# Optimization experiments

Hardware: AMD Instinct MI355X
Metric: run time of the kernel (lower is better)

The kernel has to match this reference:

```python
import jax, jax.numpy as jnp
import numpy as np
import math

EPS = 1e-5
GN_GROUPS = 32


def conv2d(x, w, padding):
    # x: [B,C,H,W], w: [O,I,kh,kw]
    return jax.lax.conv_general_dilated(
        x, w, window_strides=(1, 1), padding=[(padding, padding)] * 2,
        dimension_numbers=("NCHW", "OIHW", "NCHW"))


def group_norm(x, weight, bias, groups=GN_GROUPS, eps=EPS):
    B, C, H, W = x.shape
    xg = x.reshape(B, groups, C // groups, H, W)
    mu = xg.mean(axis=(2, 3, 4), keepdims=True)
    var = xg.var(axis=(2, 3, 4), keepdims=True)
    xn = (xg - mu) * jax.lax.rsqrt(var + eps)
    xn = xn.reshape(B, C, H, W)
    return xn * weight[None, :, None, None] + bias[None, :, None, None]


def setup_inputs() -> dict:
    key = jax.random.key(0)
    ks = jax.random.split(key, 8)
    B, C, H, W = 8, 256, 80, 80
    init_gate = 0.99
    gate_bias_val = 0.5 * math.log((1 + init_gate) / (1 - init_gate))
    return {
        "x": jax.random.normal(ks[0], (B, C, H, W), dtype=jnp.float32),
        "w1": jax.random.normal(ks[1], (C, C, 3, 3), dtype=jnp.float32) * 0.01,
        "gn1_w": jnp.ones((C,), dtype=jnp.float32),
        "gn1_b": jnp.zeros((C,), dtype=jnp.float32),
        "w2": jax.random.normal(ks[2], (C, C, 3, 3), dtype=jnp.float32) * 0.01,
        "gn2_w": jnp.ones((C,), dtype=jnp.float32),
        "gn2_b": jnp.zeros((C,), dtype=jnp.float32),
        "gate_w": jax.random.normal(ks[3], (1, C, 1, 1), dtype=jnp.float32) * 0.01,
        "gate_b": jnp.full((1,), gate_bias_val, dtype=jnp.float32),
    }


def reference(x, w1, gn1_w, gn1_b, w2, gn2_w, gn2_b, gate_w, gate_b):
    # shortcut is identity (in_channels == out_channels, stride 1)
    shortcut = x
    # conv1 -> GN -> ReLU
    h = jax.nn.relu(group_norm(conv2d(x, w1, padding=1), gn1_w, gn1_b))
    # conv2 -> GN
    h = group_norm(conv2d(h, w2, padding=1), gn2_w, gn2_b)
    # SpatialGate: 1x1 conv on the original input, ReTanH activation
    g = conv2d(x, gate_w, padding=0) + gate_b[None, :, None, None]  # [B,1,H,W]
    gate = jnp.clip(jnp.tanh(g), 0.0, None)
    # num_groups == 1: encode/decode are identity reshapes; gate broadcasts over C
    out = h * gate
    return jax.nn.relu(out + shortcut)
```

## Files before the change

kernel.cpp:

```cpp
#include <hip/hip_runtime.h>
#include <math.h>

#define NB   8
#define NC   256
#define NH   80
#define NW   80
#define NHW  6400
#define GN_EPS 1e-5f

typedef __bf16 bf16;
typedef bf16 bf16x2 __attribute__((ext_vector_type(2)));
typedef bf16 bf16x4 __attribute__((ext_vector_type(4)));
typedef bf16 bf16x8 __attribute__((ext_vector_type(8)));
typedef float f32x4 __attribute__((ext_vector_type(4)));

typedef __attribute__((address_space(1))) void gvoid;
typedef __attribute__((address_space(3))) void lvoid;
__device__ __forceinline__ void glds16(const void* g, void* l) {
    __builtin_amdgcn_global_load_lds((const gvoid*)g, (lvoid*)l, 16, 0, 0);
}

#define AW_T   2048
#define AW_BUF 18432

__global__ __launch_bounds__(256) void prep_kernel(
    const float* __restrict__ x, bf16* __restrict__ xp,
    const float* __restrict__ gw, float* __restrict__ gpart,
    const float* __restrict__ w1, const float* __restrict__ w2,
    bf16* __restrict__ wA1, bf16* __restrict__ wA2, float* __restrict__ stats)
{
    int bid = blockIdx.x;
    int tid = threadIdx.x;
    if (bid >= 5120) {
        int blk = bid - 5120;
        if (blk == 0) {
            #pragma unroll
            for (int k = 0; k < 8; k++) stats[tid + k * 256] = 0.0f;
            return;
        }
        int rb = blk - 1;
        const float* w = (rb < 2304) ? w1 : w2;
        bf16* wA       = (rb < 2304) ? wA1 : wA2;
        int idx = (rb % 2304) * 256 + tid;
        int c8  = idx & 7;
        int n   = (idx >> 3) & 15;
        int qq  = (idx >> 7) & 3;
        int coq = (idx >> 9) & 15;
        int tc  = idx >> 13;
        int tap = tc % 9, chunk = tc / 9;
        int ci = chunk * 32 + qq * 8 + c8;
        int co = coq * 16 + n;
        wA[idx] = (bf16)w[(size_t)(co * 256 + ci) * 9 + tap];
        return;
    }
    __shared__ float tile[8][4][84];
    int rg  = bid % 20;
    int cib = (bid / 20) & 31;
    int b   = bid / 640;
    for (int e = tid; e < 2560; e += 256) {
        int c8 = e / 320, r2 = e - c8 * 320;
        int rr = r2 / 80, col = r2 - rr * 80;
        tile[c8][rr][col] =
            x[((size_t)(b * NC + cib * 8 + c8) * NH + rg * 4 + rr) * NW + col];
    }
    __syncthreads();
    for (int t = tid; t < 1280; t += 256) {
        int rr = t / 320, t2 = t - rr * 320;
        int e = 2 * t2, col = e >> 3, c8 = e & 7;
        bf16x2 pk = { (bf16)tile[c8][rr][col], (bf16)tile[c8 + 1][rr][col] };
        size_t base = (((size_t)(b * 32 + cib) * 82 + rg * 4 + rr + 1) * 82) * 8 + 8;
        *(bf16x2*)(xp + base + e) = pk;
    }
    if (tid < 320) {
        int rr = tid / 80, col = tid - rr * 80;
        float s = 0.0f;
        #pragma unroll
        for (int c8 = 0; c8 < 8; c8++)
            s = fmaf(tile[c8][rr][col], gw[cib * 8 + c8], s);
        gpart[((size_t)cib * NB + b) * NHW + (rg * 4 + rr) * 80 + col] = s;
    }
    const uint4 z4 = make_uint4(0u, 0u, 0u, 0u);
    size_t img = ((size_t)(b * 32 + cib)) * 82;
    if (tid < 8) {
        int rr = tid >> 1, col = (tid & 1) * 81;
        *(uint4*)(xp + ((img + rg * 4 + rr + 1) * 82 + col) * 8) = z4;
    }
    if (rg == 0 || rg == 19) {
        int prow = (rg == 0) ? 0 : 81;
        for (int u = tid; u < 82; u += 256)
            *(uint4*)(xp + ((img + prow) * 82 + u) * 8) = z4;
    }
}

__global__ __launch_bounds__(256, 2) void conv_kernel(
    const bf16* __restrict__ xp, const bf16* __restrict__ wA,
    bf16* __restrict__ y, float* __restrict__ ssum, float* __restrict__ ssq)
{
    __shared__ __align__(16) bf16 Aw[2 * AW_BUF];
    __shared__ float wgs[8], wgq[8];

    int tid  = threadIdx.x;
    int wid  = tid >> 6;
    int lane = tid & 63;
    int n = lane & 15, q = lane >> 4;

    int bid = blockIdx.x;
    int ct  = bid / 160;
    int t   = bid - ct * 160;
    int b   = t / 20;
    int rt  = t - b * 20;
    int co0 = ct * 64, h0 = rt * 4;

    if (tid < 8) { wgs[tid] = 0.0f; wgq[tid] = 0.0f; }

    f32x4 acc[4][5];
    #pragma unroll
    for (int i = 0; i < 4; i++)
        #pragma unroll
        for (int j = 0; j < 5; j++) acc[i][j] = (f32x4){0.f, 0.f, 0.f, 0.f};

    for (int p = wid; p < 36; p += 4) {
        int tap = p >> 2, mt = p & 3;
        glds16((const char*)(wA + (((size_t)0 * 9 + tap) * 16 + ct * 4 + mt) * 512) + lane * 16,
               (char*)(Aw + tap * AW_T + mt * 512) + lane * 16);
    }

    for (int c = 0; c < 8; c++) {
        __syncthreads();
        const bf16* awc = Aw + ((c & 1) ? AW_BUF : 0) + lane * 8;
        const bf16* xq  = xp + (((size_t)(b * 32 + c * 4 + q) * 82 + (h0 + wid)) * 82) * 8 + n * 8;

        bf16x8 L0[15], L1[15];
        #pragma unroll
        for (int k = 0; k < 15; k++)
            L0[k] = *(const bf16x8*)(xq + ((k / 3) * 16 + (k % 3)) * 8);
        #pragma unroll
        for (int k = 0; k < 15; k++)
            L1[k] = *(const bf16x8*)(xq + (82 + (k / 3) * 16 + (k % 3)) * 8);

        #pragma unroll
        for (int s = 0; s < 3; s++) {
            bf16x8 af[4];
            #pragma unroll
            for (int mt = 0; mt < 4; mt++)
                af[mt] = *(const bf16x8*)(awc + s * AW_T + mt * 512);
            #pragma unroll
            for (int mt = 0; mt < 4; mt++)
                #pragma unroll
                for (int nt = 0; nt < 5; nt++)
                    acc[mt][nt] = __builtin_amdgcn_mfma_f32_16x16x32_bf16(
                        af[mt], L0[nt * 3 + s], acc[mt][nt], 0, 0, 0);
        }
        #pragma unroll
        for (int k = 0; k < 15; k++)
            L0[k] = *(const bf16x8*)(xq + (164 + (k / 3) * 16 + (k % 3)) * 8);

        __builtin_amdgcn_sched_barrier(0);

        if (c < 7) {
            bf16* dst = Aw + (((c + 1) & 1) ? AW_BUF : 0);
            for (int p = wid; p < 36; p += 4) {
                int tap = p >> 2, mt = p & 3;
                glds16((const char*)(wA + (((size_t)(c + 1) * 9 + tap) * 16 + ct * 4 + mt) * 512) + lane * 16,
                       (char*)(dst + tap * AW_T + mt * 512) + lane * 16);
            }
        }

        #pragma unroll
        for (int s = 0; s < 3; s++) {
            bf16x8 af[4];
            #pragma unroll
            for (int mt = 0; mt < 4; mt++)
                af[mt] = *(const bf16x8*)(awc + (3 + s) * AW_T + mt * 512);
            #pragma unroll
            for (int mt = 0; mt < 4; mt++)
                #pragma unroll
                for (int nt = 0; nt < 5; nt++)
                    acc[mt][nt] = __builtin_amdgcn_mfma_f32_16x16x32_bf16(
                        af[mt], L1[nt * 3 + s], acc[mt][nt], 0, 0, 0);
        }
        #pragma unroll
        for (int s = 0; s < 3; s++) {
            bf16x8 af[4];
            #pragma unroll
            for (int mt = 0; mt < 4; mt++)
                af[mt] = *(const bf16x8*)(awc + (6 + s) * AW_T + mt * 512);
            #pragma unroll
            for (int mt = 0; mt < 4; mt++)
                #pragma unroll
                for (int nt = 0; nt < 5; nt++)
                    acc[mt][nt] = __builtin_amdgcn_mfma_f32_16x16x32_bf16(
                        af[mt], L0[nt * 3 + s], acc[mt][nt], 0, 0, 0);
        }
    }

    int h = h0 + wid;
    #pragma unroll
    for (int mt = 0; mt < 4; mt++) {
        float s1 = 0.0f, s2 = 0.0f;
        int co  = co0 + mt * 16 + q * 4;
        int cib = co >> 3, c8 = co & 7;
        #pragma unroll
        for (int nt = 0; nt < 5; nt++) {
            int col = nt * 16 + n;
            bf16x4 pk;
            #pragma unroll
            for (int rg = 0; rg < 4; rg++) {
                float v = acc[mt][nt][rg];
                pk[rg] = (bf16)v;
                s1 += v;
                s2 = fmaf(v, v, s2);
            }
            *(bf16x4*)(y + ((((size_t)(b * 32 + cib) * 80 + h) * 80 + col) * 8 + c8)) = pk;
        }
        #pragma unroll
        for (int off = 1; off < 16; off <<= 1) {
            s1 += __shfl_xor(s1, off, 64);
            s2 += __shfl_xor(s2, off, 64);
        }
        if (n == 0) {
            int gl = mt * 2 + (q >> 1);
            atomicAdd(&wgs[gl], s1);
            atomicAdd(&wgq[gl], s2);
        }
    }
    __syncthreads();
    if (tid < 8) {
        atomicAdd(&ssum[b * 32 + ct * 8 + tid], wgs[tid]);
        atomicAdd(&ssq [b * 32 + ct * 8 + tid], wgq[tid]);
    }
}

__global__ __launch_bounds__(256) void prep2_kernel(
    const bf16* __restrict__ y, bf16* __restrict__ xp,
    const float* __restrict__ s, const float* __restrict__ sq,
    const float* __restrict__ gamma, const float* __restrict__ beta,
    const float* __restrict__ gpart, const float* __restrict__ gb,
    float* __restrict__ gate)
{
    int bid = blockIdx.x;
    if (bid >= 5120) {
        int i = (bid - 5120) * 256 + threadIdx.x;
        float gs = gb[0];
        #pragma unroll 8
        for (int k = 0; k < 32; k++) gs += gpart[(size_t)k * (NB * NHW) + i];
        gate[i] = fmaxf(tanhf(gs), 0.0f);
        return;
    }
    int b = bid / 640; int rem = bid - b * 640;
    int cib = rem / 20; int rq = rem - cib * 20;
    int gidx = b * 32 + cib;
    const float cnt = (float)(8 * NHW);
    float m  = s[gidx] / cnt;
    float vv = sq[gidx] / cnt - m * m;
    float r  = rsqrtf(vv + GN_EPS);
    const bf16* src = y + (size_t)(b * 32 + cib) * 51200 + rq * 2560;
    for (int u = threadIdx.x; u < 1280; u += 256) {
        int e = 2 * u;
        int row = rq * 4 + e / 640;
        int w640 = e % 640;
        int c8 = e & 7;
        int c = cib * 8 + c8;
        float sc0 = r * gamma[c],     sh0 = beta[c]     - m * sc0;
        float sc1 = r * gamma[c + 1], sh1 = beta[c + 1] - m * sc1;
        bf16x2 iv = *(const bf16x2*)(src + e);
        bf16x2 pk = { (bf16)fmaxf(fmaf((float)iv[0], sc0, sh0), 0.0f),
                      (bf16)fmaxf(fmaf((float)iv[1], sc1, sh1), 0.0f) };
        size_t xidx = (((size_t)(b * 32 + cib) * 82 + row + 1) * 82) * 8 + 8 + w640;
        *(bf16x2*)(xp + xidx) = pk;
    }
}

__global__ __launch_bounds__(256) void final_kernel(
    const bf16* __restrict__ y, const float* __restrict__ x,
    const float* __restrict__ gate,
    const float* __restrict__ s, const float* __restrict__ sq,
    const float* __restrict__ gamma, const float* __restrict__ beta,
    float* __restrict__ out)
{
    __shared__ float lds[8 * 324];
    int bid = blockIdx.x;
    int b = bid / 640; int rem = bid - b * 640;
    int cib = rem / 20; int rq = rem - cib * 20;
    int gidx = b * 32 + cib;
    const float cnt = (float)(8 * NHW);
    float m  = s[gidx] / cnt;
    float vv = sq[gidx] / cnt - m * m;
    float r  = rsqrtf(vv + GN_EPS);
    const bf16* src = y + (size_t)(b * 32 + cib) * 51200 + rq * 2560;
    for (int u = threadIdx.x; u < 1280; u += 256) {
        int e = 2 * u;
        int c8 = e & 7;
        int rc = e >> 3;
        int c = cib * 8 + c8;
        float sc0 = r * gamma[c],     sh0 = beta[c]     - m * sc0;
        float sc1 = r * gamma[c + 1], sh1 = beta[c + 1] - m * sc1;
        bf16x2 iv = *(const bf16x2*)(src + e);
        lds[c8 * 324 + rc]       = fmaf((float)iv[0], sc0, sh0);
        lds[(c8 + 1) * 324 + rc] = fmaf((float)iv[1], sc1, sh1);
    }
    __syncthreads();
    const float* gp = gate + b * NHW + rq * 320;
    for (int e2 = threadIdx.x; e2 < 2560; e2 += 256) {
        int c8 = e2 / 320, rc = e2 - c8 * 320;
        int c = cib * 8 + c8;
        size_t oidx = (size_t)(b * NC + c) * NHW + rq * 320 + rc;
        float v = fmaf(lds[c8 * 324 + rc], gp[rc], x[oidx]);
        out[oidx] = fmaxf(v, 0.0f);
    }
}

extern "C" void kernel_launch(void* const* d_in, const int* in_sizes, int n_in,
                              void* d_out, int out_size, void* d_ws, size_t ws_size,
                              hipStream_t stream)
{
    const float* x     = (const float*)d_in[0];
    const float* w1    = (const float*)d_in[1];
    const float* gn1_w = (const float*)d_in[2];
    const float* gn1_b = (const float*)d_in[3];
    const float* w2    = (const float*)d_in[4];
    const float* gn2_w = (const float*)d_in[5];
    const float* gn2_b = (const float*)d_in[6];
    const float* gw    = (const float*)d_in[7];
    const float* gb    = (const float*)d_in[8];

    bf16*  xp    = (bf16*)d_out;
    float* gpart = (float*)((char*)d_out + 27541504);
    float* out   = (float*)d_out;

    char* wsb = (char*)d_ws;
    bf16*  y     = (bf16*)wsb;
    float* gate  = (float*)(wsb + 26214400);
    bf16*  wA1   = (bf16*)(wsb + 26214400 + 204800);
    bf16*  wA2   = wA1 + 589824;
    float* stats = (float*)(wsb + 26214400 + 204800 + 2 * 1179648);
    float* s1  = stats,        * s1q = stats + 256;
    float* s2  = stats + 1024, * s2q = stats + 1280;

    prep_kernel<<<9729, 256, 0, stream>>>(x, xp, gw, gpart, w1, w2, wA1, wA2, stats);
    conv_kernel<<<640, 256, 0, stream>>>(xp, wA1, y, s1, s1q);
    prep2_kernel<<<5320, 256, 0, stream>>>(y, xp, s1, s1q, gn1_w, gn1_b, gpart, gb, gate);
    conv_kernel<<<640, 256, 0, stream>>>(xp, wA2, y, s2, s2q);
    final_kernel<<<5120, 256, 0, stream>>>(y, x, gate, s2, s2q, gn2_w, gn2_b, out);
}
```

Measured before the change: 300.7 us.

## Drop LDS weight staging in conv, vectorize prep, GN and final kernels

The conv kernel stops double-buffering weights in LDS through global_load_lds. Each wave now reads its weight fragments straight from global memory, relying on cache. This removes the per-chunk barriers and the LDS footprint, and raises launch bounds to 4 blocks per CU for higher occupancy. Prep, GN-apply and final kernels switch to wide float4/bf16x8 loads and stores, with per-channel scale and shift hoisted out of the loop. The direct weight reads add global and L2 traffic, and the conv may stall on load latency without the prefetch overlap.

New measurement: 365.5 us. 1.22x slower.

```diff
diff --git a/kernel.cpp b/kernel.cpp
--- a/kernel.cpp
+++ b/kernel.cpp
@@ -14,14 +14,6 @@
 typedef bf16 bf16x8 __attribute__((ext_vector_type(8)));
 typedef float f32x4 __attribute__((ext_vector_type(4)));
 
-typedef __attribute__((address_space(1))) void gvoid;
-typedef __attribute__((address_space(3))) void lvoid;
-__device__ __forceinline__ void glds16(const void* g, void* l) {
-    __builtin_amdgcn_global_load_lds((const gvoid*)g, (lvoid*)l, 16, 0, 0);
-}
-
-#define AW_T   2048
-#define AW_BUF 18432
 
 __global__ __launch_bounds__(256) void prep_kernel(
     const float* __restrict__ x, bf16* __restrict__ xp,
@@ -53,23 +45,25 @@
         wA[idx] = (bf16)w[(size_t)(co * 256 + ci) * 9 + tap];
         return;
     }
-    __shared__ float tile[8][4][84];
+    __shared__ float tile[8][4][88];
     int rg  = bid % 20;
     int cib = (bid / 20) & 31;
     int b   = bid / 640;
-    for (int e = tid; e < 2560; e += 256) {
-        int c8 = e / 320, r2 = e - c8 * 320;
-        int rr = r2 / 80, col = r2 - rr * 80;
-        tile[c8][rr][col] =
-            x[((size_t)(b * NC + cib * 8 + c8) * NH + rg * 4 + rr) * NW + col];
+    for (int u = tid; u < 640; u += 256) {
+        int c8 = u / 80; int rem = u - c8 * 80;
+        int rr = rem / 20; int c4 = rem - rr * 20;
+        float4 v = *(const float4*)(
+            x + ((size_t)(b * NC + cib * 8 + c8) * NH + rg * 4 + rr) * NW + c4 * 4);
+        *(float4*)(&tile[c8][rr][c4 * 4]) = v;
     }
     __syncthreads();
-    for (int t = tid; t < 1280; t += 256) {
-        int rr = t / 320, t2 = t - rr * 320;
-        int e = 2 * t2, col = e >> 3, c8 = e & 7;
-        bf16x2 pk = { (bf16)tile[c8][rr][col], (bf16)tile[c8 + 1][rr][col] };
+    for (int u = tid; u < 320; u += 256) {
+        int rr = u / 80, col = u - rr * 80;
+        bf16x8 pk;
+        #pragma unroll
+        for (int j = 0; j < 8; j++) pk[j] = (bf16)tile[j][rr][col];
         size_t base = (((size_t)(b * 32 + cib) * 82 + rg * 4 + rr + 1) * 82) * 8 + 8;
-        *(bf16x2*)(xp + base + e) = pk;
+        *(bf16x8*)(xp + base + col * 8) = pk;
     }
     if (tid < 320) {
         int rr = tid / 80, col = tid - rr * 80;
@@ -92,11 +86,10 @@
     }
 }
 
-__global__ __launch_bounds__(256, 2) void conv_kernel(
+__global__ __launch_bounds__(256, 4) void conv_kernel(
     const bf16* __restrict__ xp, const bf16* __restrict__ wA,
     bf16* __restrict__ y, float* __restrict__ ssum, float* __restrict__ ssq)
 {
-    __shared__ __align__(16) bf16 Aw[2 * AW_BUF];
     __shared__ float wgs[8], wgq[8];
 
     int tid  = threadIdx.x;
@@ -112,6 +105,7 @@
     int co0 = ct * 64, h0 = rt * 4;
 
     if (tid < 8) { wgs[tid] = 0.0f; wgq[tid] = 0.0f; }
+    __syncthreads();
 
     f32x4 acc[4][5];
     #pragma unroll
@@ -119,16 +113,11 @@
         #pragma unroll
         for (int j = 0; j < 5; j++) acc[i][j] = (f32x4){0.f, 0.f, 0.f, 0.f};
 
-    for (int p = wid; p < 36; p += 4) {
-        int tap = p >> 2, mt = p & 3;
-        glds16((const char*)(wA + (((size_t)0 * 9 + tap) * 16 + ct * 4 + mt) * 512) + lane * 16,
-               (char*)(Aw + tap * AW_T + mt * 512) + lane * 16);
-    }
+    const bf16* wAl = wA + (size_t)ct * 2048 + lane * 8;
 
     for (int c = 0; c < 8; c++) {
-        __syncthreads();
-        const bf16* awc = Aw + ((c & 1) ? AW_BUF : 0) + lane * 8;
-        const bf16* xq  = xp + (((size_t)(b * 32 + c * 4 + q) * 82 + (h0 + wid)) * 82) * 8 + n * 8;
+        const bf16* wc = wAl + (size_t)c * 73728;
+        const bf16* xq = xp + (((size_t)(b * 32 + c * 4 + q) * 82 + (h0 + wid)) * 82) * 8 + n * 8;
 
         bf16x8 L0[15], L1[15];
         #pragma unroll
@@ -143,7 +132,7 @@
             bf16x8 af[4];
             #pragma unroll
             for (int mt = 0; mt < 4; mt++)
-                af[mt] = *(const bf16x8*)(awc + s * AW_T + mt * 512);
+                af[mt] = *(const bf16x8*)(wc + s * 8192 + mt * 512);
             #pragma unroll
             for (int mt = 0; mt < 4; mt++)
                 #pragma unroll
@@ -155,23 +144,12 @@
         for (int k = 0; k < 15; k++)
             L0[k] = *(const bf16x8*)(xq + (164 + (k / 3) * 16 + (k % 3)) * 8);
 
-        __builtin_amdgcn_sched_barrier(0);
-
-        if (c < 7) {
-            bf16* dst = Aw + (((c + 1) & 1) ? AW_BUF : 0);
-            for (int p = wid; p < 36; p += 4) {
-                int tap = p >> 2, mt = p & 3;
-                glds16((const char*)(wA + (((size_t)(c + 1) * 9 + tap) * 16 + ct * 4 + mt) * 512) + lane * 16,
-                       (char*)(dst + tap * AW_T + mt * 512) + lane * 16);
-            }
-        }
-
         #pragma unroll
         for (int s = 0; s < 3; s++) {
             bf16x8 af[4];
             #pragma unroll
             for (int mt = 0; mt < 4; mt++)
-                af[mt] = *(const bf16x8*)(awc + (3 + s) * AW_T + mt * 512);
+                af[mt] = *(const bf16x8*)(wc + (3 + s) * 8192 + mt * 512);
             #pragma unroll
             for (int mt = 0; mt < 4; mt++)
                 #pragma unroll
@@ -184,7 +162,7 @@
             bf16x8 af[4];
             #pragma unroll
             for (int mt = 0; mt < 4; mt++)
-                af[mt] = *(const bf16x8*)(awc + (6 + s) * AW_T + mt * 512);
+                af[mt] = *(const bf16x8*)(wc + (6 + s) * 8192 + mt * 512);
             #pragma unroll
             for (int mt = 0; mt < 4; mt++)
                 #pragma unroll
@@ -254,20 +232,25 @@
     float m  = s[gidx] / cnt;
     float vv = sq[gidx] / cnt - m * m;
     float r  = rsqrtf(vv + GN_EPS);
+    float scj[8], shj[8];
+    #pragma unroll
+    for (int j = 0; j < 8; j++) {
+        int c = cib * 8 + j;
+        scj[j] = r * gamma[c];
+        shj[j] = beta[c] - m * scj[j];
+    }
     const bf16* src = y + (size_t)(b * 32 + cib) * 51200 + rq * 2560;
-    for (int u = threadIdx.x; u < 1280; u += 256) {
-        int e = 2 * u;
+    for (int u = threadIdx.x; u < 320; u += 256) {
+        int e = u * 8;
         int row = rq * 4 + e / 640;
-        int w640 = e % 640;
-        int c8 = e & 7;
-        int c = cib * 8 + c8;
-        float sc0 = r * gamma[c],     sh0 = beta[c]     - m * sc0;
-        float sc1 = r * gamma[c + 1], sh1 = beta[c + 1] - m * sc1;
-        bf16x2 iv = *(const bf16x2*)(src + e);
-        bf16x2 pk = { (bf16)fmaxf(fmaf((float)iv[0], sc0, sh0), 0.0f),
-                      (bf16)fmaxf(fmaf((float)iv[1], sc1, sh1), 0.0f) };
+        int w640 = e - (e / 640) * 640;
+        bf16x8 iv = *(const bf16x8*)(src + e);
+        bf16x8 pk;
+        #pragma unroll
+        for (int j = 0; j < 8; j++)
+            pk[j] = (bf16)fmaxf(fmaf((float)iv[j], scj[j], shj[j]), 0.0f);
         size_t xidx = (((size_t)(b * 32 + cib) * 82 + row + 1) * 82) * 8 + 8 + w640;
-        *(bf16x2*)(xp + xidx) = pk;
+        *(bf16x8*)(xp + xidx) = pk;
     }
 }
 
@@ -278,7 +261,7 @@
     const float* __restrict__ gamma, const float* __restrict__ beta,
     float* __restrict__ out)
 {
-    __shared__ float lds[8 * 324];
+    __shared__ float lds[8 * 328];
     int bid = blockIdx.x;
     int b = bid / 640; int rem = bid - b * 640;
     int cib = rem / 20; int rq = rem - cib * 20;
@@ -287,26 +270,35 @@
     float m  = s[gidx] / cnt;
     float vv = sq[gidx] / cnt - m * m;
     float r  = rsqrtf(vv + GN_EPS);
+    float scj[8], shj[8];
+    #pragma unroll
+    for (int j = 0; j < 8; j++) {
+        int c = cib * 8 + j;
+        scj[j] = r * gamma[c];
+        shj[j] = beta[c] - m * scj[j];
+    }
     const bf16* src = y + (size_t)(b * 32 + cib) * 51200 + rq * 2560;
-    for (int u = threadIdx.x; u < 1280; u += 256) {
-        int e = 2 * u;
-        int c8 = e & 7;
-        int rc = e >> 3;
-        int c = cib * 8 + c8;
-        float sc0 = r * gamma[c],     sh0 = beta[c]     - m * sc0;
-        float sc1 = r * gamma[c + 1], sh1 = beta[c + 1] - m * sc1;
-        bf16x2 iv = *(const bf16x2*)(src + e);
-        lds[c8 * 324 + rc]       = fmaf((float)iv[0], sc0, sh0);
-        lds[(c8 + 1) * 324 + rc] = fmaf((float)iv[1], sc1, sh1);
+    for (int u = threadIdx.x; u < 320; u += 256) {
+        bf16x8 iv = *(const bf16x8*)(src + u * 8);
+        #pragma unroll
+        for (int j = 0; j < 8; j++)
+            lds[j * 328 + u] = fmaf((float)iv[j], scj[j], shj[j]);
     }
     __syncthreads();
     const float* gp = gate + b * NHW + rq * 320;
-    for (int e2 = threadIdx.x; e2 < 2560; e2 += 256) {
-        int c8 = e2 / 320, rc = e2 - c8 * 320;
+    for (int u = threadIdx.x; u < 640; u += 256) {
+        int c8 = u / 80; int rc = (u - c8 * 80) * 4;
         int c = cib * 8 + c8;
         size_t oidx = (size_t)(b * NC + c) * NHW + rq * 320 + rc;
-        float v = fmaf(lds[c8 * 324 + rc], gp[rc], x[oidx]);
-        out[oidx] = fmaxf(v, 0.0f);
+        float4 xv = *(const float4*)(x + oidx);
+        float4 gv = *(const float4*)(gp + rc);
+        float4 lv = *(const float4*)(&lds[c8 * 328 + rc]);
+        float4 ov;
+        ov.x = fmaxf(fmaf(lv.x, gv.x, xv.x), 0.0f);
+        ov.y = fmaxf(fmaf(lv.y, gv.y, xv.y), 0.0f);
+        ov.z = fmaxf(fmaf(lv.z, gv.z, xv.z), 0.0f);
+        ov.w = fmaxf(fmaf(lv.w, gv.w, xv.w), 0.0f);
+        *(float4*)(out + oidx) = ov;
     }
 }
 
```
